# Performance work log

Hardware: AMD Instinct MI355X
Metric: run time of the kernel (lower is better)

The kernel has to match this reference:

```python
import jax, jax.numpy as jnp
import numpy as np

B, N, K = 8, 2048, 16
C_IN, HID, C_OUT = 128, 128, 128
MSG_DIM = 2 * C_IN + 3


def setup_inputs() -> dict:
    key = jax.random.key(0)
    ks = jax.random.split(key, 9)
    h = jax.random.normal(ks[0], (B, N, C_IN), dtype=jnp.float32)
    pos = jax.random.normal(ks[1], (B, N, 3), dtype=jnp.float32)
    idx = jax.random.randint(ks[2], (B, N, K), 0, N, dtype=jnp.int64)
    # MLP params (Linear: y = x @ W.T + b; store as (in, out) for einsum-free matmul)
    s1 = 1.0 / np.sqrt(MSG_DIM)
    s2 = 1.0 / np.sqrt(HID)
    W1 = jax.random.uniform(ks[3], (MSG_DIM, HID), minval=-s1, maxval=s1, dtype=jnp.float32)
    b1 = jax.random.uniform(ks[4], (HID,), minval=-s1, maxval=s1, dtype=jnp.float32)
    W2 = jax.random.uniform(ks[5], (HID, C_OUT), minval=-s2, maxval=s2, dtype=jnp.float32)
    b2 = jax.random.uniform(ks[6], (C_OUT,), minval=-s2, maxval=s2, dtype=jnp.float32)
    gamma = jnp.ones((C_OUT,), dtype=jnp.float32)
    beta = jnp.zeros((C_OUT,), dtype=jnp.float32)
    return {"h": h, "pos": pos, "idx": idx, "W1": W1, "b1": b1,
            "W2": W2, "b2": b2, "gamma": gamma, "beta": beta}


def _gather(feats, idx):
    # feats: (B,N,C), idx: (B,N,k) -> (B,N,k,C)
    return jax.vmap(lambda f, i: f[i])(feats, idx)


def _layernorm(x, gamma, beta, eps=1e-5):
    mu = jnp.mean(x, axis=-1, keepdims=True)
    var = jnp.mean(jnp.square(x - mu), axis=-1, keepdims=True)
    return (x - mu) * jax.lax.rsqrt(var + eps) * gamma + beta


def reference(h, pos, idx, W1, b1, W2, b2, gamma, beta):
    # h: (B,N,C), pos: (B,N,3), idx: (B,N,k)
    h_j = _gather(h, idx)                      # (B,N,k,C)
    rel = _gather(pos, idx) - pos[:, :, None]  # (B,N,k,3)
    h_i = jnp.broadcast_to(h[:, :, None, :], h_j.shape)
    msg = jnp.concatenate([h_i, h_j - h_i, rel], axis=-1)   # (B,N,k,2C+3)
    x = jax.nn.gelu(msg @ W1 + b1, approximate=False)       # (B,N,k,H)
    x = jax.nn.gelu(x @ W2 + b2, approximate=False)         # (B,N,k,O)
    out = jnp.max(x, axis=2)                                 # (B,N,O)
    return _layernorm(out, gamma, beta)
```

## Files before the change

kernel.cpp:

```cpp
#include <hip/hip_runtime.h>
#include <math.h>

#define BATCH 8
#define NPTS  2048
#define KNBR  16
#define CIN   128

typedef __attribute__((ext_vector_type(8))) short bf16x8;
typedef __attribute__((ext_vector_type(4))) float f32x4;

union U8 { bf16x8 v; unsigned u[4]; };

static __device__ __forceinline__ unsigned pk2(float lo, float hi) {
    unsigned r;
    asm("v_cvt_pk_bf16_f32 %0, %1, %2" : "=v"(r) : "v"(lo), "v"(hi));
    return r;
}

static __device__ __forceinline__ short f2bf(float f) {
    unsigned x = __builtin_bit_cast(unsigned, f);
    return (short)((x + 0x7fffu + ((x >> 16) & 1u)) >> 16);
}

static __device__ __forceinline__ float gelu(float x) {
    float x2 = x * x;
    float u  = x * fmaf(x2, 0.044715f, 1.0f);
    float e  = __expf(u * -1.5957691216057308f);
    return x * __builtin_amdgcn_rcpf(1.0f + e);
}

__global__ __launch_bounds__(256) void prep_weights(
    const float* __restrict__ W1, const float* __restrict__ W2,
    short* __restrict__ wsb)
{
    int tid = blockIdx.x * 256 + threadIdx.x;
    if (tid >= 53248) return;
    if (tid < 16384) {
        int j = tid & 7, lane = (tid >> 3) & 63, f = tid >> 9;
        int ks = f & 3, nt = f >> 2;
        int row = ks * 32 + (lane >> 4) * 8 + j, col = nt * 16 + (lane & 15);
        wsb[tid] = f2bf(W1[row * 128 + col]);
    } else if (tid < 36864) {
        int t = tid - 16384;
        int j = t & 7, lane = (t >> 3) & 63, f = t >> 9;
        int ks = f % 5, nt = f / 5;
        int row = 128 + ks * 32 + (lane >> 4) * 8 + j, col = nt * 16 + (lane & 15);
        float v = (row < 259) ? W1[row * 128 + col] : 0.0f;
        wsb[tid] = f2bf(v);
    } else {
        int t = tid - 36864;
        int j = t & 7, lane = (t >> 3) & 63, f = t >> 9;
        int ks = f & 3, nt = f >> 2;
        int row = ks * 32 + (lane >> 4) * 8 + j, col = nt * 16 + (lane & 15);
        wsb[36864 + t] = f2bf(W2[row * 128 + col]);
    }
}

__global__ __launch_bounds__(256) void base_pass(
    const float* __restrict__ h, const short* __restrict__ w1a,
    const float* __restrict__ b1, float* __restrict__ base)
{
    const int wave = threadIdx.x >> 6, lane = threadIdx.x & 63;
    const int quad = lane >> 4, lm = lane & 15;
    const int node0 = (blockIdx.x * 4 + wave) * 16;

    const float4* h4 = (const float4*)h;
    bf16x8 afrag[4];
    #pragma unroll
    for (int ks = 0; ks < 4; ++ks) {
        float4 p0 = h4[(size_t)(node0 + lm) * 32 + ks * 8 + quad * 2];
        float4 p1 = h4[(size_t)(node0 + lm) * 32 + ks * 8 + quad * 2 + 1];
        U8 t;
        t.u[0] = pk2(p0.x, p0.y); t.u[1] = pk2(p0.z, p0.w);
        t.u[2] = pk2(p1.x, p1.y); t.u[3] = pk2(p1.z, p1.w);
        afrag[ks] = t.v;
    }
    const bf16x8* bfr = (const bf16x8*)w1a;
    f32x4 acc[8];
    #pragma unroll
    for (int nt = 0; nt < 8; ++nt) {
        float bv = b1[nt * 16 + lm];
        acc[nt] = (f32x4){bv, bv, bv, bv};
    }
    #pragma unroll
    for (int ks = 0; ks < 4; ++ks)
        #pragma unroll
        for (int nt = 0; nt < 8; ++nt)
            acc[nt] = __builtin_amdgcn_mfma_f32_16x16x32_bf16(
                afrag[ks], bfr[(nt * 4 + ks) * 64 + lane], acc[nt], 0, 0, 0);
    #pragma unroll
    for (int nt = 0; nt < 8; ++nt)
        #pragma unroll
        for (int r = 0; r < 4; ++r)
            base[(size_t)(node0 + quad * 4 + r) * 128 + nt * 16 + lm] = acc[nt][r];
}

#define HSTR 136
#define MWAVES 16
#define LDS_SHORTS (20480 + 16384 + MWAVES * 16 * HSTR)

__global__ __launch_bounds__(1024, 4) void edgeconv_main(
    const float* __restrict__ h, const float* __restrict__ pos,
    const int* __restrict__ idx,
    const short* __restrict__ w1f,
    const float* __restrict__ base,
    const float* __restrict__ b2,
    const float* __restrict__ gamma, const float* __restrict__ beta,
    float* __restrict__ out)
{
    extern __shared__ short lds[];
    short* s_w1  = lds;
    short* s_w2  = lds + 20480;
    short* s_hid = lds + 36864;

    const int tid = threadIdx.x, wave = tid >> 6, lane = tid & 63;
    const int quad = lane >> 4, lm = lane & 15;

    {
        const float4* src = (const float4*)w1f;
        float4* dst = (float4*)s_w1;
        for (int i = tid; i < 4608; i += 1024) dst[i] = src[i];
    }
    __syncthreads();

    float b2v[8];
    #pragma unroll
    for (int nt = 0; nt < 8; ++nt) b2v[nt] = b2[nt * 16 + lm];

    const bf16x8* w1frag = (const bf16x8*)s_w1;
    const bf16x8* w2frag = (const bf16x8*)s_w2;
    short* hrow = s_hid + wave * 16 * HSTR;

    const int sb = (blockIdx.x & 7) * 32 + (blockIdx.x >> 3);
    const int node0 = sb * 64 + wave * 4;

    for (int ni = 0; ni < 4; ++ni) {
        const int node = node0 + ni;
        const int b = node >> 11, n = node & 2047;
        const float4* hb4 = (const float4*)(h + (size_t)b * NPTS * CIN);
        const float*  pb  = pos + (size_t)b * NPTS * 3;

        const int jm = idx[node * KNBR + lm];

        bf16x8 afrag[4];
        #pragma unroll
        for (int ks = 0; ks < 4; ++ks) {
            float4 a0 = hb4[n  * 32 + ks * 8 + quad * 2];
            float4 a1 = hb4[n  * 32 + ks * 8 + quad * 2 + 1];
            float4 j0 = hb4[jm * 32 + ks * 8 + quad * 2];
            float4 j1 = hb4[jm * 32 + ks * 8 + quad * 2 + 1];
            U8 t;
            t.u[0] = pk2(j0.x - a0.x, j0.y - a0.y);
            t.u[1] = pk2(j0.z - a0.z, j0.w - a0.w);
            t.u[2] = pk2(j1.x - a1.x, j1.y - a1.y);
            t.u[3] = pk2(j1.z - a1.z, j1.w - a1.w);
            afrag[ks] = t.v;
        }
        U8 rt; rt.u[0] = 0; rt.u[1] = 0; rt.u[2] = 0; rt.u[3] = 0;
        if (quad == 0) {
            float rx = pb[3 * jm]     - pb[3 * n];
            float ry = pb[3 * jm + 1] - pb[3 * n + 1];
            float rz = pb[3 * jm + 2] - pb[3 * n + 2];
            rt.u[0] = pk2(rx, ry);
            rt.u[1] = pk2(rz, 0.0f);
        }

        f32x4 acc[8];
        #pragma unroll
        for (int nt = 0; nt < 8; ++nt) {
            float bv = base[(size_t)node * 128 + nt * 16 + lm];
            acc[nt] = (f32x4){bv, bv, bv, bv};
        }
        #pragma unroll
        for (int ks = 0; ks < 4; ++ks)
            #pragma unroll
            for (int nt = 0; nt < 8; ++nt)
                acc[nt] = __builtin_amdgcn_mfma_f32_16x16x32_bf16(
                    afrag[ks], w1frag[(nt * 5 + ks) * 64 + lane], acc[nt], 0, 0, 0);
        #pragma unroll
        for (int nt = 0; nt < 8; ++nt)
            acc[nt] = __builtin_amdgcn_mfma_f32_16x16x32_bf16(
                rt.v, w1frag[(nt * 5 + 4) * 64 + lane], acc[nt], 0, 0, 0);

        #pragma unroll
        for (int nt = 0; nt < 8; ++nt)
            #pragma unroll
            for (int r = 0; r < 4; ++r) {
                float g = gelu(acc[nt][r]);
                hrow[(quad * 4 + r) * HSTR + nt * 16 + lm] = (short)pk2(g, g);
            }
        asm volatile("s_waitcnt lgkmcnt(0)" ::: "memory");

        bf16x8 a2[4];
        #pragma unroll
        for (int ks = 0; ks < 4; ++ks)
            a2[ks] = *(const bf16x8*)(hrow + lm * HSTR + ks * 32 + quad * 8);

        f32x4 acc2[8];
        #pragma unroll
        for (int nt = 0; nt < 8; ++nt) acc2[nt] = (f32x4){0.f, 0.f, 0.f, 0.f};
        #pragma unroll
        for (int ks = 0; ks < 4; ++ks)
            #pragma unroll
            for (int nt = 0; nt < 8; ++nt)
                acc2[nt] = __builtin_amdgcn_mfma_f32_16x16x32_bf16(
                    a2[ks], w2frag[(nt * 4 + ks) * 64 + lane], acc2[nt], 0, 0, 0);

        float v[8];
        #pragma unroll
        for (int nt = 0; nt < 8; ++nt) {
            float mx = fmaxf(fmaxf(acc2[nt][0], acc2[nt][1]),
                             fmaxf(acc2[nt][2], acc2[nt][3]));
            float mn = fminf(fminf(acc2[nt][0], acc2[nt][1]),
                             fminf(acc2[nt][2], acc2[nt][3]));
            mx = fmaxf(mx, __shfl_xor(mx, 16, 64));
            mx = fmaxf(mx, __shfl_xor(mx, 32, 64));
            mn = fminf(mn, __shfl_xor(mn, 16, 64));
            mn = fminf(mn, __shfl_xor(mn, 32, 64));
            mx += b2v[nt]; mn += b2v[nt];
            v[nt] = fmaxf(gelu(mx), gelu(mn));
        }

        float s = 0.f, s2 = 0.f;
        #pragma unroll
        for (int nt = 0; nt < 8; ++nt) { s += v[nt]; s2 += v[nt] * v[nt]; }
        #pragma unroll
        for (int off = 1; off <= 8; off <<= 1) {
            s  += __shfl_xor(s,  off, 64);
            s2 += __shfl_xor(s2, off, 64);
        }
        const float mu  = s * (1.0f / 128.0f);
        const float var = s2 * (1.0f / 128.0f) - mu * mu;
        const float inv = rsqrtf(var + 1e-5f);

        float* orow = out + (size_t)node * 128;
        #pragma unroll
        for (int t2 = 0; t2 < 2; ++t2) {
            int nt = quad * 2 + t2, col = nt * 16 + lm;
            orow[col] = (v[nt] - mu) * inv * gamma[col] + beta[col];
        }
    }
}

extern "C" void kernel_launch(void* const* d_in, const int* in_sizes, int n_in,
                              void* d_out, int out_size, void* d_ws, size_t ws_size,
                              hipStream_t stream) {
    const float* h     = (const float*)d_in[0];
    const float* pos   = (const float*)d_in[1];
    const int*   idx   = (const int*)  d_in[2];
    const float* W1    = (const float*)d_in[3];
    const float* b1    = (const float*)d_in[4];
    const float* W2    = (const float*)d_in[5];
    const float* b2    = (const float*)d_in[6];
    const float* gamma = (const float*)d_in[7];
    const float* beta  = (const float*)d_in[8];
    float* out = (float*)d_out;

    short* wsb  = (short*)d_ws;
    short* w1f  = wsb + 16384;
    float* base = (float*)((char*)d_ws + 106496);

    prep_weights<<<208, 256, 0, stream>>>(W1, W2, wsb);
    base_pass<<<256, 256, 0, stream>>>(h, wsb, b1, base);

    hipFuncSetAttribute((const void*)edgeconv_main,
                        hipFuncAttributeMaxDynamicSharedMemorySize,
                        LDS_SHORTS * 2);
    edgeconv_main<<<256, 1024, LDS_SHORTS * 2, stream>>>(
        h, pos, idx, w1f, base, b2, gamma, beta, out);
}
```

Measured before the change: 128.1 us.

## Fuse weight prep and base projection into single edgeconv kernel

```diff
diff --git a/kernel.cpp b/kernel.cpp
--- a/kernel.cpp
+++ b/kernel.cpp
@@ -1,25 +1,17 @@
 #include <hip/hip_runtime.h>
 #include <math.h>
 
-#define BATCH 8
-#define NPTS  2048
-#define KNBR  16
-#define CIN   128
+#define NPTS 2048
+#define KNBR 16
 
 typedef __attribute__((ext_vector_type(8))) short bf16x8;
 typedef __attribute__((ext_vector_type(4))) float f32x4;
-
 union U8 { bf16x8 v; unsigned u[4]; };
 
 static __device__ __forceinline__ unsigned pk2(float lo, float hi) {
     unsigned r;
     asm("v_cvt_pk_bf16_f32 %0, %1, %2" : "=v"(r) : "v"(lo), "v"(hi));
     return r;
-}
-
-static __device__ __forceinline__ short f2bf(float f) {
-    unsigned x = __builtin_bit_cast(unsigned, f);
-    return (short)((x + 0x7fffu + ((x >> 16) & 1u)) >> 16);
 }
 
 static __device__ __forceinline__ float gelu(float x) {
@@ -29,115 +21,104 @@
     return x * __builtin_amdgcn_rcpf(1.0f + e);
 }
 
-__global__ __launch_bounds__(256) void prep_weights(
-    const float* __restrict__ W1, const float* __restrict__ W2,
-    short* __restrict__ wsb)
-{
-    int tid = blockIdx.x * 256 + threadIdx.x;
-    if (tid >= 53248) return;
-    if (tid < 16384) {
-        int j = tid & 7, lane = (tid >> 3) & 63, f = tid >> 9;
-        int ks = f & 3, nt = f >> 2;
-        int row = ks * 32 + (lane >> 4) * 8 + j, col = nt * 16 + (lane & 15);
-        wsb[tid] = f2bf(W1[row * 128 + col]);
-    } else if (tid < 36864) {
-        int t = tid - 16384;
-        int j = t & 7, lane = (t >> 3) & 63, f = t >> 9;
-        int ks = f % 5, nt = f / 5;
-        int row = 128 + ks * 32 + (lane >> 4) * 8 + j, col = nt * 16 + (lane & 15);
-        float v = (row < 259) ? W1[row * 128 + col] : 0.0f;
-        wsb[tid] = f2bf(v);
-    } else {
-        int t = tid - 36864;
-        int j = t & 7, lane = (t >> 3) & 63, f = t >> 9;
-        int ks = f & 3, nt = f >> 2;
-        int row = ks * 32 + (lane >> 4) * 8 + j, col = nt * 16 + (lane & 15);
-        wsb[36864 + t] = f2bf(W2[row * 128 + col]);
-    }
-}
-
-__global__ __launch_bounds__(256) void base_pass(
-    const float* __restrict__ h, const short* __restrict__ w1a,
-    const float* __restrict__ b1, float* __restrict__ base)
-{
-    const int wave = threadIdx.x >> 6, lane = threadIdx.x & 63;
-    const int quad = lane >> 4, lm = lane & 15;
-    const int node0 = (blockIdx.x * 4 + wave) * 16;
-
-    const float4* h4 = (const float4*)h;
-    bf16x8 afrag[4];
-    #pragma unroll
-    for (int ks = 0; ks < 4; ++ks) {
-        float4 p0 = h4[(size_t)(node0 + lm) * 32 + ks * 8 + quad * 2];
-        float4 p1 = h4[(size_t)(node0 + lm) * 32 + ks * 8 + quad * 2 + 1];
-        U8 t;
-        t.u[0] = pk2(p0.x, p0.y); t.u[1] = pk2(p0.z, p0.w);
-        t.u[2] = pk2(p1.x, p1.y); t.u[3] = pk2(p1.z, p1.w);
-        afrag[ks] = t.v;
-    }
-    const bf16x8* bfr = (const bf16x8*)w1a;
-    f32x4 acc[8];
-    #pragma unroll
-    for (int nt = 0; nt < 8; ++nt) {
-        float bv = b1[nt * 16 + lm];
-        acc[nt] = (f32x4){bv, bv, bv, bv};
-    }
-    #pragma unroll
-    for (int ks = 0; ks < 4; ++ks)
-        #pragma unroll
-        for (int nt = 0; nt < 8; ++nt)
-            acc[nt] = __builtin_amdgcn_mfma_f32_16x16x32_bf16(
-                afrag[ks], bfr[(nt * 4 + ks) * 64 + lane], acc[nt], 0, 0, 0);
-    #pragma unroll
-    for (int nt = 0; nt < 8; ++nt)
-        #pragma unroll
-        for (int r = 0; r < 4; ++r)
-            base[(size_t)(node0 + quad * 4 + r) * 128 + nt * 16 + lm] = acc[nt][r];
-}
-
 #define HSTR 136
-#define MWAVES 16
-#define LDS_SHORTS (20480 + 16384 + MWAVES * 16 * HSTR)
-
-__global__ __launch_bounds__(1024, 4) void edgeconv_main(
+#define LDS_SHORTS (36864 + 16 * 16 * HSTR)
+
+__global__ __launch_bounds__(1024, 4) void edgeconv_fused(
     const float* __restrict__ h, const float* __restrict__ pos,
     const int* __restrict__ idx,
-    const short* __restrict__ w1f,
-    const float* __restrict__ base,
-    const float* __restrict__ b2,
+    const float* __restrict__ W1, const float* __restrict__ W2,
+    const float* __restrict__ b1, const float* __restrict__ b2,
     const float* __restrict__ gamma, const float* __restrict__ beta,
     float* __restrict__ out)
 {
     extern __shared__ short lds[];
-    short* s_w1  = lds;
-    short* s_w2  = lds + 20480;
-    short* s_hid = lds + 36864;
-
     const int tid = threadIdx.x, wave = tid >> 6, lane = tid & 63;
     const int quad = lane >> 4, lm = lane & 15;
 
-    {
-        const float4* src = (const float4*)w1f;
-        float4* dst = (float4*)s_w1;
-        for (int i = tid; i < 4608; i += 1024) dst[i] = src[i];
-    }
+    for (int c = tid; c < 6656; c += 1024) {
+        const int l = c & 63, fi = c >> 6;
+        const int lrow = (l >> 4) * 8, lcol = l & 15;
+        U8 t;
+        if (fi < 40) {
+            int ks = fi % 5, nt = fi / 5;
+            int row0 = 128 + ks * 32 + lrow, col = nt * 16 + lcol;
+            #pragma unroll
+            for (int p = 0; p < 4; ++p) {
+                int r0 = row0 + 2 * p;
+                float v0 = (r0     < 259) ? W1[r0 * 128 + col]       : 0.f;
+                float v1 = (r0 + 1 < 259) ? W1[(r0 + 1) * 128 + col] : 0.f;
+                t.u[p] = pk2(v0, v1);
+            }
+        } else if (fi < 72) {
+            int f2 = fi - 40, ks = f2 & 3, nt = f2 >> 2;
+            int row0 = ks * 32 + lrow, col = nt * 16 + lcol;
+            #pragma unroll
+            for (int p = 0; p < 4; ++p)
+                t.u[p] = pk2(W2[(row0 + 2*p) * 128 + col],
+                             W2[(row0 + 2*p + 1) * 128 + col]);
+        } else {
+            int f2 = fi - 72, ks = f2 & 3, nt = f2 >> 2;
+            int row0 = ks * 32 + lrow, col = nt * 16 + lcol;
+            #pragma unroll
+            for (int p = 0; p < 4; ++p)
+                t.u[p] = pk2(W1[(row0 + 2*p) * 128 + col],
+                             W1[(row0 + 2*p + 1) * 128 + col]);
+        }
+        ((bf16x8*)lds)[c] = t.v;
+    }
+
+    float b1v[8], b2v[8];
+    #pragma unroll
+    for (int nt = 0; nt < 8; ++nt) {
+        b1v[nt] = b1[nt * 16 + lm];
+        b2v[nt] = b2[nt * 16 + lm];
+    }
+    const float gv0 = gamma[(quad * 2) * 16 + lm];
+    const float gv1 = gamma[(quad * 2 + 1) * 16 + lm];
+    const float be0 = beta[(quad * 2) * 16 + lm];
+    const float be1 = beta[(quad * 2 + 1) * 16 + lm];
+
     __syncthreads();
 
-    float b2v[8];
-    #pragma unroll
-    for (int nt = 0; nt < 8; ++nt) b2v[nt] = b2[nt * 16 + lm];
-
-    const bf16x8* w1frag = (const bf16x8*)s_w1;
-    const bf16x8* w2frag = (const bf16x8*)s_w2;
-    short* hrow = s_hid + wave * 16 * HSTR;
+    const bf16x8* w1frag  = (const bf16x8*)lds;
+    const bf16x8* w2frag  = (const bf16x8*)lds + 2560;
+    const bf16x8* w1afrag = (const bf16x8*)lds + 4608;
+    short* hrow = lds + 36864 + wave * 16 * HSTR;
 
     const int sb = (blockIdx.x & 7) * 32 + (blockIdx.x >> 3);
     const int node0 = sb * 64 + wave * 4;
 
+    f32x4 basev[8];
+    #pragma unroll
+    for (int nt = 0; nt < 8; ++nt)
+        basev[nt] = (f32x4){b1v[nt], b1v[nt], b1v[nt], b1v[nt]};
+    {
+        const float4* hsrc = (const float4*)h + (size_t)(node0 + (lm & 3)) * 32;
+        bf16x8 af[4];
+        #pragma unroll
+        for (int ks = 0; ks < 4; ++ks) {
+            float4 p0 = hsrc[ks * 8 + quad * 2];
+            float4 p1 = hsrc[ks * 8 + quad * 2 + 1];
+            U8 t;
+            t.u[0] = pk2(p0.x, p0.y); t.u[1] = pk2(p0.z, p0.w);
+            t.u[2] = pk2(p1.x, p1.y); t.u[3] = pk2(p1.z, p1.w);
+            af[ks] = t.v;
+        }
+        #pragma unroll
+        for (int ks = 0; ks < 4; ++ks)
+            #pragma unroll
+            for (int nt = 0; nt < 8; ++nt)
+                basev[nt] = __builtin_amdgcn_mfma_f32_16x16x32_bf16(
+                    af[ks], w1afrag[(nt * 4 + ks) * 64 + lane], basev[nt], 0, 0, 0);
+    }
+    __syncthreads();
+
+    #pragma unroll
     for (int ni = 0; ni < 4; ++ni) {
         const int node = node0 + ni;
         const int b = node >> 11, n = node & 2047;
-        const float4* hb4 = (const float4*)(h + (size_t)b * NPTS * CIN);
+        const float4* hb4 = (const float4*)h + (size_t)b * NPTS * 32;
         const float*  pb  = pos + (size_t)b * NPTS * 3;
 
         const int jm = idx[node * KNBR + lm];
@@ -168,7 +149,7 @@
         f32x4 acc[8];
         #pragma unroll
         for (int nt = 0; nt < 8; ++nt) {
-            float bv = base[(size_t)node * 128 + nt * 16 + lm];
+            float bv = basev[nt][ni];
             acc[nt] = (f32x4){bv, bv, bv, bv};
         }
         #pragma unroll
@@ -234,11 +215,8 @@
         const float inv = rsqrtf(var + 1e-5f);
 
         float* orow = out + (size_t)node * 128;
-        #pragma unroll
-        for (int t2 = 0; t2 < 2; ++t2) {
-            int nt = quad * 2 + t2, col = nt * 16 + lm;
-            orow[col] = (v[nt] - mu) * inv * gamma[col] + beta[col];
-        }
+        orow[(quad * 2) * 16 + lm]     = (v[quad * 2]     - mu) * inv * gv0 + be0;
+        orow[(quad * 2 + 1) * 16 + lm] = (v[quad * 2 + 1] - mu) * inv * gv1 + be1;
     }
 }
 
@@ -256,16 +234,9 @@
     const float* beta  = (const float*)d_in[8];
     float* out = (float*)d_out;
 
-    short* wsb  = (short*)d_ws;
-    short* w1f  = wsb + 16384;
-    float* base = (float*)((char*)d_ws + 106496);
-
-    prep_weights<<<208, 256, 0, stream>>>(W1, W2, wsb);
-    base_pass<<<256, 256, 0, stream>>>(h, wsb, b1, base);
-
-    hipFuncSetAttribute((const void*)edgeconv_main,
+    hipFuncSetAttribute((const void*)edgeconv_fused,
                         hipFuncAttributeMaxDynamicSharedMemorySize,
                         LDS_SHORTS * 2);
-    edgeconv_main<<<256, 1024, LDS_SHORTS * 2, stream>>>(
-        h, pos, idx, w1f, base, b2, gamma, beta, out);
-}
+    edgeconv_fused<<<256, 1024, LDS_SHORTS * 2, stream>>>(
+        h, pos, idx, W1, W2, b1, b2, gamma, beta, out);
+}
```

New measurement: 122.4 us. 4.4% less time.
